# Kernel optimization log

Hardware: AMD Instinct MI355X
Metric: run time of the kernel (lower is better)

## Reference

```python
import jax, jax.numpy as jnp
import numpy as np

B, V, D = 1024, 50000, 300
EPS = 1e-7


def setup_inputs() -> dict:
    key = jax.random.key(0)
    k1, k2 = jax.random.split(key)
    # soft multi-hot label mask over the vocab (torch code multiplies floats)
    labels = jax.random.uniform(k1, (B, V), dtype=jnp.float32)
    # pretrained word2vec-style embedding table
    weight = jax.random.normal(k2, (V, D), dtype=jnp.float32)
    return {"labels": labels, "weight": weight}


def reference(labels, weight):
    # torch: mul(weight, labels[:, :, None]).sum(1)  ==  labels @ weight
    attr = jnp.einsum('bv,vd->bd', labels, weight)  # (B, D)
    # L2 normalize: attr / (sqrt(sum(attr^2, 1)) + 1e-7)
    norm = jnp.sqrt(jnp.sum(attr * attr, axis=1, keepdims=True))
    return attr / (norm + EPS)
```

## Files before the change

### kernel.cpp

```cpp
#include <hip/hip_runtime.h>
#include <hip/hip_bf16.h>
#include <math.h>

typedef __bf16 bf16;
typedef bf16 bf16x8 __attribute__((ext_vector_type(8)));
typedef float f32x4 __attribute__((ext_vector_type(4)));

constexpr int Mdim = 1024;
constexpr int Kdim = 50000;
constexpr int Ndim = 300;
constexpr int NP   = 320;

constexpr int BM = 64, BN = 320, BK = 64;
constexpr int BKP = 72;
constexpr int MT = Mdim / BM;
constexpr int SPLIT = 16;
constexpr int SEGLEN = 3136;

__device__ __forceinline__ bf16x8 bzero8() {
    bf16x8 v;
#pragma unroll
    for (int e = 0; e < 8; ++e) v[e] = (bf16)0.0f;
    return v;
}

constexpr int TK = 64;
__global__ __launch_bounds__(256) void transpose_w(const float* __restrict__ W,
                                                   bf16* __restrict__ Wt)
{
    __shared__ bf16 tile[NP * BKP];
    const int k0 = blockIdx.x * TK;
    const int t  = threadIdx.x;

    for (int c = t; c < 64 * 75; c += 256) {
        const int kk = c / 75;
        const int ch = c % 75;
        const int k  = k0 + kk;
        float4 v = make_float4(0.f, 0.f, 0.f, 0.f);
        if (k < Kdim) v = *(const float4*)(W + (size_t)k * Ndim + ch * 4);
        const int n = ch * 4;
        tile[(n + 0) * BKP + kk] = (bf16)v.x;
        tile[(n + 1) * BKP + kk] = (bf16)v.y;
        tile[(n + 2) * BKP + kk] = (bf16)v.z;
        tile[(n + 3) * BKP + kk] = (bf16)v.w;
    }
    __syncthreads();
    for (int c = t; c < NP * 8; c += 256) {
        const int n  = c >> 3;
        const int ch = c & 7;
        const int k  = k0 + ch * 8;
        if (k + 8 <= Kdim) {
            bf16x8 v;
            if (n < Ndim) v = *(const bf16x8*)(&tile[n * BKP + ch * 8]);
            else          v = bzero8();
            *(bf16x8*)(Wt + (size_t)n * Kdim + k) = v;
        }
    }
}

__global__ __launch_bounds__(512) void gemm_kernel(const float* __restrict__ A,
                                                   const bf16* __restrict__ Wt,
                                                   float* __restrict__ Cacc)
{
    __shared__ bf16 As[BM * BKP];
    __shared__ bf16 Bs[BN * BKP];

    const int bx   = blockIdx.x;
    const int mt   = bx & (MT - 1);
    const int ks   = bx >> 4;
    const int m0   = mt * BM;
    const int kbeg = ks * SEGLEN;
    const int kend = min(kbeg + SEGLEN, Kdim);

    const int t    = threadIdx.x;
    const int lane = t & 63;
    const int wave = t >> 6;
    const int wm   = wave >> 2;
    const int wn   = wave & 3;
    const int lm   = lane & 15;
    const int lq   = lane >> 4;

    const int arow = t >> 3;
    const int acol = (t & 7) * 8;
    const float* aptr = A + (size_t)(m0 + arow) * Kdim;

    f32x4 acc[2][5] = {};

    for (int k0 = kbeg; k0 < kend; k0 += BK) {
        __syncthreads();
        {
            const int k = k0 + acol;
            bf16x8 v = bzero8();
            if (k + 8 <= kend) {
                float4 f0 = *(const float4*)(aptr + k);
                float4 f1 = *(const float4*)(aptr + k + 4);
                v[0] = (bf16)f0.x; v[1] = (bf16)f0.y; v[2] = (bf16)f0.z; v[3] = (bf16)f0.w;
                v[4] = (bf16)f1.x; v[5] = (bf16)f1.y; v[6] = (bf16)f1.z; v[7] = (bf16)f1.w;
            }
            *(bf16x8*)(&As[arow * BKP + acol]) = v;
        }
#pragma unroll
        for (int i = 0; i < 5; ++i) {
            const int c    = t + 512 * i;
            const int brow = c >> 3;
            const int bcol = (c & 7) * 8;
            const int k    = k0 + bcol;
            bf16x8 v = bzero8();
            if (k + 8 <= kend)
                v = *(const bf16x8*)(Wt + (size_t)brow * Kdim + k);
            *(bf16x8*)(&Bs[brow * BKP + bcol]) = v;
        }
        __syncthreads();
#pragma unroll
        for (int s = 0; s < 2; ++s) {
            bf16x8 a[2], b[5];
#pragma unroll
            for (int i = 0; i < 2; ++i)
                a[i] = *(const bf16x8*)(&As[(wm * 32 + i * 16 + lm) * BKP + s * 32 + lq * 8]);
#pragma unroll
            for (int j = 0; j < 5; ++j)
                b[j] = *(const bf16x8*)(&Bs[(wn * 80 + j * 16 + lm) * BKP + s * 32 + lq * 8]);
#pragma unroll
            for (int i = 0; i < 2; ++i)
#pragma unroll
                for (int j = 0; j < 5; ++j)
                    acc[i][j] = __builtin_amdgcn_mfma_f32_16x16x32_bf16(a[i], b[j], acc[i][j], 0, 0, 0);
        }
    }

    const int col0 = wn * 80 + lm;
    const int row0 = m0 + wm * 32 + lq * 4;
#pragma unroll
    for (int i = 0; i < 2; ++i)
#pragma unroll
        for (int j = 0; j < 5; ++j)
#pragma unroll
            for (int r = 0; r < 4; ++r)
                atomicAdd(&Cacc[(size_t)(row0 + i * 16 + r) * NP + col0 + j * 16],
                          acc[i][j][r]);
}

__global__ __launch_bounds__(320) void normalize_k(const float* __restrict__ Cacc,
                                                   float* __restrict__ out)
{
    const int b = blockIdx.x;
    const int t = threadIdx.x;
    float v = 0.f;
    if (t < Ndim) v = Cacc[(size_t)b * NP + t];
    float ss = v * v;
#pragma unroll
    for (int o = 32; o > 0; o >>= 1) ss += __shfl_down(ss, o, 64);
    __shared__ float wsum[5];
    __shared__ float scale;
    if ((t & 63) == 0) wsum[t >> 6] = ss;
    __syncthreads();
    if (t == 0) {
        float s = wsum[0] + wsum[1] + wsum[2] + wsum[3] + wsum[4];
        scale = 1.0f / (sqrtf(s) + 1e-7f);
    }
    __syncthreads();
    if (t < Ndim) out[(size_t)b * Ndim + t] = v * scale;
}

extern "C" void kernel_launch(void* const* d_in, const int* in_sizes, int n_in,
                              void* d_out, int out_size, void* d_ws, size_t ws_size,
                              hipStream_t stream)
{
    const float* labels = (const float*)d_in[0];
    const float* weight = (const float*)d_in[1];
    float* out = (float*)d_out;

    float* Cacc = (float*)d_ws;
    bf16*  Wt   = (bf16*)((char*)d_ws + (size_t)Mdim * NP * sizeof(float));

    hipMemsetAsync(Cacc, 0, (size_t)Mdim * NP * sizeof(float), stream);
    transpose_w<<<dim3((Kdim + TK - 1) / TK), dim3(256), 0, stream>>>(weight, Wt);
    gemm_kernel<<<dim3(MT * SPLIT), dim3(512), 0, stream>>>(labels, Wt, Cacc);
    normalize_k<<<dim3(Mdim), dim3(320), 0, stream>>>(Cacc, out);
}
```

Before: 423.2 us.

## Prefetch GEMM tiles into registers, enlarge M tile, rework transpose LDS layout

The GEMM now loads the next K-tile from global memory into registers while the MFMAs run on the current LDS tile, overlapping memory latency with compute. The M tile grows from 64 to 128 rows with split-K raised to 32, so each block reuses each W tile across more rows and the grid stays at 256 blocks. The transpose kernel stores the tile row-major with an odd stride of 301 to cut LDS bank conflicts on the writes, then gathers columns element by element when reading. The costs are more registers (acc grows to 4x5, plus prefetch buffers), an extra barrier per iteration, and twice as many atomic adds into the accumulator.

```diff
diff --git a/kernel.cpp b/kernel.cpp
--- a/kernel.cpp
+++ b/kernel.cpp
@@ -11,11 +11,11 @@
 constexpr int Ndim = 300;
 constexpr int NP   = 320;
 
-constexpr int BM = 64, BN = 320, BK = 64;
+constexpr int BM = 128, BN = 320, BK = 64;
 constexpr int BKP = 72;
 constexpr int MT = Mdim / BM;
-constexpr int SPLIT = 16;
-constexpr int SEGLEN = 3136;
+constexpr int SPLIT = 32;
+constexpr int SEGLEN = 1600;
 
 __device__ __forceinline__ bf16x8 bzero8() {
     bf16x8 v;
@@ -25,10 +25,11 @@
 }
 
 constexpr int TK = 64;
+constexpr int TS = 301;
 __global__ __launch_bounds__(256) void transpose_w(const float* __restrict__ W,
                                                    bf16* __restrict__ Wt)
 {
-    __shared__ bf16 tile[NP * BKP];
+    __shared__ bf16 tile[TK * TS];
     const int k0 = blockIdx.x * TK;
     const int t  = threadIdx.x;
 
@@ -38,11 +39,8 @@
         const int k  = k0 + kk;
         float4 v = make_float4(0.f, 0.f, 0.f, 0.f);
         if (k < Kdim) v = *(const float4*)(W + (size_t)k * Ndim + ch * 4);
-        const int n = ch * 4;
-        tile[(n + 0) * BKP + kk] = (bf16)v.x;
-        tile[(n + 1) * BKP + kk] = (bf16)v.y;
-        tile[(n + 2) * BKP + kk] = (bf16)v.z;
-        tile[(n + 3) * BKP + kk] = (bf16)v.w;
+        bf16* p = &tile[kk * TS + ch * 4];
+        p[0] = (bf16)v.x; p[1] = (bf16)v.y; p[2] = (bf16)v.z; p[3] = (bf16)v.w;
     }
     __syncthreads();
     for (int c = t; c < NP * 8; c += 256) {
@@ -50,9 +48,11 @@
         const int ch = c & 7;
         const int k  = k0 + ch * 8;
         if (k + 8 <= Kdim) {
-            bf16x8 v;
-            if (n < Ndim) v = *(const bf16x8*)(&tile[n * BKP + ch * 8]);
-            else          v = bzero8();
+            bf16x8 v = bzero8();
+            if (n < Ndim) {
+#pragma unroll
+                for (int j = 0; j < 8; ++j) v[j] = tile[(ch * 8 + j) * TS + n];
+            }
             *(bf16x8*)(Wt + (size_t)n * Kdim + k) = v;
         }
     }
@@ -67,7 +67,7 @@
 
     const int bx   = blockIdx.x;
     const int mt   = bx & (MT - 1);
-    const int ks   = bx >> 4;
+    const int ks   = bx >> 3;
     const int m0   = mt * BM;
     const int kbeg = ks * SEGLEN;
     const int kend = min(kbeg + SEGLEN, Kdim);
@@ -80,58 +80,76 @@
     const int lm   = lane & 15;
     const int lq   = lane >> 4;
 
-    const int arow = t >> 3;
-    const int acol = (t & 7) * 8;
+    const int arow = t >> 2;
+    const int acol = (t & 3) * 16;
     const float* aptr = A + (size_t)(m0 + arow) * Kdim;
 
-    f32x4 acc[2][5] = {};
+    float4 af[4];
+    bf16x8 bfr[5];
 
-    for (int k0 = kbeg; k0 < kend; k0 += BK) {
-        __syncthreads();
-        {
-            const int k = k0 + acol;
-            bf16x8 v = bzero8();
-            if (k + 8 <= kend) {
-                float4 f0 = *(const float4*)(aptr + k);
-                float4 f1 = *(const float4*)(aptr + k + 4);
-                v[0] = (bf16)f0.x; v[1] = (bf16)f0.y; v[2] = (bf16)f0.z; v[3] = (bf16)f0.w;
-                v[4] = (bf16)f1.x; v[5] = (bf16)f1.y; v[6] = (bf16)f1.z; v[7] = (bf16)f1.w;
-            }
-            *(bf16x8*)(&As[arow * BKP + acol]) = v;
+    auto load_tiles = [&](int k0) {
+#pragma unroll
+        for (int i = 0; i < 4; ++i) {
+            const int k = k0 + acol + i * 4;
+            af[i] = (k + 4 <= kend) ? *(const float4*)(aptr + k)
+                                    : make_float4(0.f, 0.f, 0.f, 0.f);
         }
 #pragma unroll
         for (int i = 0; i < 5; ++i) {
-            const int c    = t + 512 * i;
+            const int c = t + 512 * i;
             const int brow = c >> 3;
             const int bcol = (c & 7) * 8;
-            const int k    = k0 + bcol;
-            bf16x8 v = bzero8();
-            if (k + 8 <= kend)
-                v = *(const bf16x8*)(Wt + (size_t)brow * Kdim + k);
-            *(bf16x8*)(&Bs[brow * BKP + bcol]) = v;
+            const int k = k0 + bcol;
+            bfr[i] = (k + 8 <= kend) ? *(const bf16x8*)(Wt + (size_t)brow * Kdim + k)
+                                     : bzero8();
         }
+    };
+    auto store_tiles = [&]() {
+        bf16x8 v0, v1;
+        v0[0]=(bf16)af[0].x; v0[1]=(bf16)af[0].y; v0[2]=(bf16)af[0].z; v0[3]=(bf16)af[0].w;
+        v0[4]=(bf16)af[1].x; v0[5]=(bf16)af[1].y; v0[6]=(bf16)af[1].z; v0[7]=(bf16)af[1].w;
+        v1[0]=(bf16)af[2].x; v1[1]=(bf16)af[2].y; v1[2]=(bf16)af[2].z; v1[3]=(bf16)af[2].w;
+        v1[4]=(bf16)af[3].x; v1[5]=(bf16)af[3].y; v1[6]=(bf16)af[3].z; v1[7]=(bf16)af[3].w;
+        *(bf16x8*)(&As[arow * BKP + acol])     = v0;
+        *(bf16x8*)(&As[arow * BKP + acol + 8]) = v1;
+#pragma unroll
+        for (int i = 0; i < 5; ++i) {
+            const int c = t + 512 * i;
+            const int brow = c >> 3;
+            const int bcol = (c & 7) * 8;
+            *(bf16x8*)(&Bs[brow * BKP + bcol]) = bfr[i];
+        }
+    };
+
+    f32x4 acc[4][5] = {};
+
+    load_tiles(kbeg);
+    for (int k0 = kbeg; k0 < kend; k0 += BK) {
+        store_tiles();
         __syncthreads();
+        if (k0 + BK < kend) load_tiles(k0 + BK);
 #pragma unroll
         for (int s = 0; s < 2; ++s) {
-            bf16x8 a[2], b[5];
+            bf16x8 a[4], b[5];
 #pragma unroll
-            for (int i = 0; i < 2; ++i)
-                a[i] = *(const bf16x8*)(&As[(wm * 32 + i * 16 + lm) * BKP + s * 32 + lq * 8]);
+            for (int i = 0; i < 4; ++i)
+                a[i] = *(const bf16x8*)(&As[(wm * 64 + i * 16 + lm) * BKP + s * 32 + lq * 8]);
 #pragma unroll
             for (int j = 0; j < 5; ++j)
                 b[j] = *(const bf16x8*)(&Bs[(wn * 80 + j * 16 + lm) * BKP + s * 32 + lq * 8]);
 #pragma unroll
-            for (int i = 0; i < 2; ++i)
+            for (int i = 0; i < 4; ++i)
 #pragma unroll
                 for (int j = 0; j < 5; ++j)
                     acc[i][j] = __builtin_amdgcn_mfma_f32_16x16x32_bf16(a[i], b[j], acc[i][j], 0, 0, 0);
         }
+        __syncthreads();
     }
 
     const int col0 = wn * 80 + lm;
-    const int row0 = m0 + wm * 32 + lq * 4;
+    const int row0 = m0 + wm * 64 + lq * 4;
 #pragma unroll
-    for (int i = 0; i < 2; ++i)
+    for (int i = 0; i < 4; ++i)
 #pragma unroll
         for (int j = 0; j < 5; ++j)
 #pragma unroll
```

Result: faster. 392.0 us (-7.4%).
